# Kernel optimization log

Measured on AMD Instinct MI355X. Metric: run time of the kernel, lower is better.

The kernel has to match this reference:

```python
import jax, jax.numpy as jnp
import numpy as np

B = 32           # graphs in batch
N_PER = 512      # nodes per graph
N = B * N_PER    # 16384 total nodes (block-diagonal batched graph)
E = N * 16       # 262144 edges
D_IN = 128
D_OUT = 128
ASSIGN = 2048    # total clusters = B * K
K = ASSIGN // B  # 64 clusters per graph


def setup_inputs() -> dict:
    key = jax.random.key(0)
    ks = jax.random.split(key, 6)
    h = jax.random.normal(ks[0], (N, D_IN), jnp.float32)
    # edges confined within each graph -> block-diagonal batched adjacency
    gid = jnp.repeat(jnp.arange(B), E // B)
    edge_src = (jax.random.randint(ks[1], (E,), 0, N_PER) + gid * N_PER).astype(jnp.int32)
    edge_dst = (jax.random.randint(ks[2], (E,), 0, N_PER) + gid * N_PER).astype(jnp.int32)
    # GraphSage NodeApply linears: Linear(2*in, out)
    stdv_f = 1.0 / np.sqrt(2 * D_IN)
    W_feat = jax.random.uniform(ks[3], (2 * D_IN, D_OUT), jnp.float32, -stdv_f, stdv_f)
    b_feat = jnp.zeros((D_OUT,), jnp.float32)
    W_pool = jax.random.uniform(ks[4], (2 * D_IN, ASSIGN), jnp.float32, -stdv_f, stdv_f)
    b_pool = jnp.zeros((ASSIGN,), jnp.float32)
    return {"h": h, "W_feat": W_feat, "b_feat": b_feat,
            "W_pool": W_pool, "b_pool": b_pool,
            "edge_src": edge_src, "edge_dst": edge_dst}


def _graphsage(h, W, b, src, dst):
    # mean aggregation over in-neighbors (dropout=0, batch_norm off)
    msg = jax.ops.segment_sum(h[src], dst, num_segments=N)          # [N, d_in]
    deg = jax.ops.segment_sum(jnp.ones((src.shape[0],), h.dtype), dst, num_segments=N)
    h_neigh = msg / jnp.maximum(deg, 1.0)[:, None]
    bundle = jnp.concatenate([h, h_neigh], axis=1) @ W + b          # [N, d_out]
    # F.normalize(p=2, dim=1) then activation, as in GraphSage NodeApply
    norm = jnp.linalg.norm(bundle, axis=1, keepdims=True)
    bundle = bundle / jnp.maximum(norm, 1e-12)
    return jax.nn.relu(bundle)


def _forward(h, W_feat, b_feat, W_pool, b_pool, src, dst):
    feat = _graphsage(h, W_feat, b_feat, src, dst)       # [N, D_OUT]
    assign = _graphsage(h, W_pool, b_pool, src, dst)     # [N, ASSIGN]
    # block-diagonal mask: node i of graph g may only assign to g's K clusters
    gid_n = jnp.arange(N) // N_PER                       # [N]
    gid_c = jnp.arange(ASSIGN) // K                      # [ASSIGN]
    mask = (gid_n[:, None] == gid_c[None, :]).astype(jnp.float32)
    # masked_softmax with memory_efficient=False
    s = jax.nn.softmax(assign * mask, axis=-1) * mask
    s = s / (s.sum(axis=-1, keepdims=True) + 1e-13)      # [N, ASSIGN]
    h_new = s.T @ feat                                   # [ASSIGN, D_OUT]
    # adj_new = S^T A S without densifying A: (A S)[dst] += S[src]
    a_s = jax.ops.segment_sum(s[src], dst, num_segments=N)
    adj_new = s.T @ a_s                                  # [ASSIGN, ASSIGN]
    return adj_new, h_new


def reference(h, W_feat, b_feat, W_pool, b_pool, edge_src, edge_dst):
    return _forward(h, W_feat, b_feat, W_pool, b_pool, edge_src, edge_dst)
```

## Files before the change

### kernel.cpp

```cpp
#include <hip/hip_runtime.h>

#define NB   32
#define NPER 512
#define NN   16384
#define EE   262144
#define DD   128
#define AS   2048
#define KC   64

using short8   = __attribute__((ext_vector_type(8))) short;
using floatx4  = __attribute__((ext_vector_type(4))) float;
using ushort4v = __attribute__((ext_vector_type(4))) unsigned short;

typedef __attribute__((address_space(3))) unsigned int lds_u32;
typedef const __attribute__((address_space(1))) unsigned int gbl_u32;

static __device__ __forceinline__ void gload16(const unsigned short* g, unsigned short* l) {
    __builtin_amdgcn_global_load_lds((gbl_u32*)g, (lds_u32*)l, 16, 0, 0);
}
static __device__ __forceinline__ float bits2f(unsigned int u) {
    union { unsigned int i; float f; } z; z.i = u << 16; return z.f;
}
static __device__ __forceinline__ unsigned short f2b(float x) {
    union { float f; unsigned int u; } v; v.f = x;
    unsigned int r = v.u + 0x7fffu + ((v.u >> 16) & 1u);
    return (unsigned short)(r >> 16);
}
static __device__ __forceinline__ unsigned short f2b_exact(float x) {
    union { float f; unsigned int u; } v; v.f = x;
    return (unsigned short)(v.u >> 16);
}

union PrepSMem {
    unsigned short fT[128 * 136];
    float tl[32][33];
    struct { unsigned short glA[4096]; unsigned short glB[4096]; float gcred[4]; } gg;
};
__global__ void prep_kernel(const float* __restrict__ h, unsigned short* __restrict__ bundle,
                            unsigned short* __restrict__ hT, const int* __restrict__ esrc,
                            const int* __restrict__ edst, unsigned int* __restrict__ Acnt,
                            const float* __restrict__ Wf, const float* __restrict__ Wp,
                            const float* __restrict__ bp,
                            unsigned short* __restrict__ WfT, unsigned short* __restrict__ WpT,
                            float* __restrict__ Gf, float* __restrict__ uF,
                            float* __restrict__ cF) {
    __shared__ PrepSMem sm;
    int b = blockIdx.x, t = threadIdx.x;
    if (b < 32) {
        int ks = b >> 2, ti = (b >> 1) & 1, tj = b & 1;
        int wv = t >> 6, lane = t & 63;
        int mw = wv >> 1, nw = wv & 1, q = lane >> 4, lm = lane & 15;
        int swz = q ^ ((lm >> 1) & 3);
        floatx4 acc[4][4];
#pragma unroll
        for (int mi = 0; mi < 4; mi++)
#pragma unroll
            for (int ni = 0; ni < 4; ni++) acc[mi][ni] = (floatx4)0.f;
        for (int ki = 0; ki < 8; ki++) {
            int k0 = ks * 256 + ki * 32;
#pragma unroll
            for (int half = 0; half < 2; half++) {
                int u = t + 256 * half;
                int row = u >> 2, c = u & 3;
                int cs = c ^ ((row >> 1) & 3);
                const float4* sa = reinterpret_cast<const float4*>(
                    Wp + (size_t)(ti * 128 + row) * 2048 + k0 + c * 8);
                float4 v0 = sa[0], v1 = sa[1];
                ushort4v p0 = { f2b(v0.x), f2b(v0.y), f2b(v0.z), f2b(v0.w) };
                ushort4v p1 = { f2b(v1.x), f2b(v1.y), f2b(v1.z), f2b(v1.w) };
                *reinterpret_cast<ushort4v*>(&sm.gg.glA[(row * 4 + cs) * 8]) = p0;
                *reinterpret_cast<ushort4v*>(&sm.gg.glA[(row * 4 + cs) * 8 + 4]) = p1;
                const float4* sb = reinterpret_cast<const float4*>(
                    Wp + (size_t)(tj * 128 + row) * 2048 + k0 + c * 8);
                float4 w0 = sb[0], w1 = sb[1];
                ushort4v q0 = { f2b(w0.x), f2b(w0.y), f2b(w0.z), f2b(w0.w) };
                ushort4v q1 = { f2b(w1.x), f2b(w1.y), f2b(w1.z), f2b(w1.w) };
                *reinterpret_cast<ushort4v*>(&sm.gg.glB[(row * 4 + cs) * 8]) = q0;
                *reinterpret_cast<ushort4v*>(&sm.gg.glB[(row * 4 + cs) * 8 + 4]) = q1;
            }
            __syncthreads();
            short8 aF[4], bF[4];
#pragma unroll
            for (int mi = 0; mi < 4; mi++)
                aF[mi] = *reinterpret_cast<const short8*>(&sm.gg.glA[((64 * mw + 16 * mi + lm) * 4 + swz) * 8]);
#pragma unroll
            for (int ni = 0; ni < 4; ni++)
                bF[ni] = *reinterpret_cast<const short8*>(&sm.gg.glB[((64 * nw + 16 * ni + lm) * 4 + swz) * 8]);
#pragma unroll
            for (int mi = 0; mi < 4; mi++)
#pragma unroll
                for (int ni = 0; ni < 4; ni++)
                    acc[mi][ni] = __builtin_amdgcn_mfma_f32_16x16x32_bf16(aF[mi], bF[ni], acc[mi][ni], 0, 0, 0);
            __syncthreads();
        }
#pragma unroll
        for (int mi = 0; mi < 4; mi++)
#pragma unroll
            for (int ni = 0; ni < 4; ni++)
#pragma unroll
                for (int r = 0; r < 4; r++)
                    atomicAdd(&Gf[(size_t)(ti * 128 + 64 * mw + 16 * mi + 4 * q + r) * 256 +
                                  tj * 128 + 64 * nw + 16 * ni + lm], acc[mi][ni][r]);
        if (tj == 0) {
            int row = t >> 1, jh = t & 1;
            const float4* wr = reinterpret_cast<const float4*>(
                Wp + (size_t)(ti * 128 + row) * 2048 + ks * 256 + jh * 128);
            const float4* br = reinterpret_cast<const float4*>(bp + ks * 256 + jh * 128);
            float s = 0.f;
#pragma unroll 8
            for (int j = 0; j < 32; j++) {
                float4 a = wr[j], c = br[j];
                s += a.x * c.x + a.y * c.y + a.z * c.z + a.w * c.w;
            }
            s += __shfl_xor(s, 1, 64);
            if (jh == 0) atomicAdd(&uF[ti * 128 + row], s);
        }
        if (b == 0) {
            float s = 0.f;
            for (int j = t; j < 2048; j += 256) { float v = bp[j]; s += v * v; }
#pragma unroll
            for (int d = 1; d < 64; d <<= 1) s += __shfl_xor(s, d, 64);
            if (lane == 0) sm.gg.gcred[wv] = s;
            __syncthreads();
            if (t == 0) atomicAdd(cF, sm.gg.gcred[0] + sm.gg.gcred[1] + sm.gg.gcred[2] + sm.gg.gcred[3]);
        }
    } else if (b < 160) {
        int node0 = (b - 32) * 128;
        int r = t >> 1, hf = t & 1;
        const float4* h4 = reinterpret_cast<const float4*>(h + (size_t)(node0 + r) * 128 + hf * 64);
        unsigned short* bo = bundle + (size_t)(node0 + r) * 256 + hf * 64;
#pragma unroll
        for (int i = 0; i < 16; i++) {
            float4 v = h4[i];
            ushort4v o = { f2b(v.x), f2b(v.y), f2b(v.z), f2b(v.w) };
            *reinterpret_cast<ushort4v*>(bo + 4 * i) = o;
            int c = hf * 64 + 4 * i;
            sm.fT[(c + 0) * 136 + r] = o.x;
            sm.fT[(c + 1) * 136 + r] = o.y;
            sm.fT[(c + 2) * 136 + r] = o.z;
            sm.fT[(c + 3) * 136 + r] = o.w;
        }
        __syncthreads();
        int c = t >> 1, nh = t & 1;
        const uint4* src = reinterpret_cast<const uint4*>(&sm.fT[c * 136 + nh * 64]);
        uint4* dst = reinterpret_cast<uint4*>(hT + (size_t)c * NN + node0 + nh * 64);
#pragma unroll
        for (int i = 0; i < 8; i++) dst[i] = src[i];
    } else if (b < 1184) {
        int e = (b - 160) * 256 + t;
        int d = edst[e], sl = esrc[e] & 511;
        int idx = d * 512 + sl;
        atomicAdd(&Acnt[idx >> 2], 1u << (8 * (idx & 3)));
    } else {
        int tb = b - 1184;
        int bx = tb % 68, by = tb / 68;
        int tx = t & 31, ty = t >> 5;
        const float* in; unsigned short* out; int C, cb;
        if (bx < DD / 32) { in = Wf; out = WfT; C = DD; cb = bx; }
        else              { in = Wp; out = WpT; C = AS; cb = bx - DD / 32; }
        int c0 = cb * 32, r0 = by * 32;
        for (int i = 0; i < 4; i++)
            sm.tl[ty + 8 * i][tx] = in[(size_t)(r0 + ty + 8 * i) * C + c0 + tx];
        __syncthreads();
        for (int i = 0; i < 4; i++)
            out[(size_t)(c0 + ty + 8 * i) * 256 + r0 + tx] = f2b(sm.tl[tx][ty + 8 * i]);
    }
}

__global__ __launch_bounds__(256) void agg_h_mfma_kernel(
    const unsigned int* __restrict__ Acnt, const unsigned short* __restrict__ hT,
    unsigned short* __restrict__ bundle, unsigned short* __restrict__ Aadj,
    const float* __restrict__ Gf, unsigned short* __restrict__ Gb) {
    __shared__ alignas(16) unsigned short lA[64 * 512];
    __shared__ float rs[64];
    int tid = threadIdx.x, bx = blockIdx.x;
    if (bx >= 256) {
        int base = (bx - 256) * 16384;
        for (int i = 0; i < 16; i++) {
            int idx = base + i * 1024 + tid * 4;
            float4 v = *reinterpret_cast<const float4*>(Gf + idx);
            ushort4v o = { f2b(v.x), f2b(v.y), f2b(v.z), f2b(v.w) };
            *reinterpret_cast<ushort4v*>(&Gb[idx]) = o;
        }
        return;
    }
    int r0 = bx * 64, g = bx >> 3;
    int wv = tid >> 6, lane = tid & 63, q = lane >> 4, lm = lane & 15;
    int mw = wv >> 1, nw = wv & 1;
    if (tid < 64) rs[tid] = 0.f;
    __syncthreads();
#pragma unroll
    for (int j = 0; j < 8; j++) {
        int ub = tid + 256 * j;
        int row = ub >> 5, kb = ub & 31;
        uint4 w = reinterpret_cast<const uint4*>(Acnt)[(size_t)(r0 + row) * 32 + kb];
        unsigned int wa[4] = { w.x, w.y, w.z, w.w };
        unsigned short ob[16];
        float sum = 0.f;
#pragma unroll
        for (int i = 0; i < 4; i++) {
#pragma unroll
            for (int bb = 0; bb < 4; bb++) {
                float fv = (float)((wa[i] >> (8 * bb)) & 0xffu);
                sum += fv;
                ob[4 * i + bb] = f2b_exact(fv);
            }
        }
        atomicAdd(&rs[row], sum);
        uint4* gdst = reinterpret_cast<uint4*>(&Aadj[(size_t)(r0 + row) * 512 + kb * 16]);
        gdst[0] = *reinterpret_cast<const uint4*>(&ob[0]);
        gdst[1] = *reinterpret_cast<const uint4*>(&ob[8]);
#pragma unroll
        for (int jj = 0; jj < 2; jj++) {
            int pos = (kb * 2 + jj) ^ (row & 7);
            *reinterpret_cast<uint4*>(&lA[(row * 64 + pos) * 8]) =
                *reinterpret_cast<const uint4*>(&ob[8 * jj]);
        }
    }
    floatx4 acc[2][4];
#pragma unroll
    for (int mt = 0; mt < 2; mt++)
#pragma unroll
        for (int nt = 0; nt < 4; nt++) acc[mt][nt] = (floatx4)0.f;
    __syncthreads();
    const unsigned short* Bb = hT + (size_t)(64 * nw + lm) * NN + g * 512 + (q << 3);
    short8 bF[2][4];
#pragma unroll
    for (int nt = 0; nt < 4; nt++)
        bF[0][nt] = *reinterpret_cast<const short8*>(Bb + (size_t)16 * nt * NN);
    for (int ki = 0; ki < 16; ki++) {
        if (ki < 15) {
#pragma unroll
            for (int nt = 0; nt < 4; nt++)
                bF[(ki + 1) & 1][nt] =
                    *reinterpret_cast<const short8*>(Bb + (size_t)16 * nt * NN + (ki + 1) * 32);
        }
        short8 aF[2];
        int swz = (4 * ki + q) ^ (lm & 7);
#pragma unroll
        for (int mt = 0; mt < 2; mt++)
            aF[mt] = *reinterpret_cast<const short8*>(&lA[((32 * mw + 16 * mt + lm) * 64 + swz) * 8]);
#pragma unroll
        for (int mt = 0; mt < 2; mt++)
#pragma unroll
            for (int nt = 0; nt < 4; nt++)
                acc[mt][nt] = __builtin_amdgcn_mfma_f32_16x16x32_bf16(aF[mt], bF[ki & 1][nt],
                                                                      acc[mt][nt], 0, 0, 0);
    }
#pragma unroll
    for (int mt = 0; mt < 2; mt++)
#pragma unroll
        for (int r = 0; r < 4; r++) {
            int row = 32 * mw + 16 * mt + 4 * q + r;
            float inv = 1.0f / fmaxf(rs[row], 1.0f);
#pragma unroll
            for (int nt = 0; nt < 4; nt++)
                bundle[(size_t)(r0 + row) * 256 + 128 + 64 * nw + 16 * nt + lm] =
                    f2b(acc[mt][nt][r] * inv);
        }
}

union FPSMem {
    struct { unsigned short lA[4096]; unsigned short lB[4096]; float red[256]; } feat;
    struct { unsigned short lA[16384]; float raw[4352]; float ssq[256]; float rn[64];
             float uL[256]; } pool;
};
__global__ __launch_bounds__(256) void featpool_kernel(
    const unsigned short* __restrict__ bundle, const unsigned short* __restrict__ WfT,
    const unsigned short* __restrict__ WpT, const unsigned short* __restrict__ Gb,
    const float* __restrict__ bfe, const float* __restrict__ bp,
    const float* __restrict__ uF, const float* __restrict__ cF,
    unsigned short* __restrict__ featT, unsigned short* __restrict__ sT) {
    __shared__ FPSMem sm;
    int tid = threadIdx.x, b = blockIdx.x;
    if (b < 128) {
        int r0 = b * 128;
        int wv = tid >> 6, lane = tid & 63;
        int mw = wv >> 1, nw = wv & 1, q = lane >> 4, lm = lane & 15;
        int rowS0 = tid >> 2,         cS0 = (tid & 3) ^ ((rowS0 >> 1) & 3);
        int rowS1 = (tid + 256) >> 2, cS1 = ((tid + 256) & 3) ^ ((rowS1 >> 1) & 3);
        int swz = q ^ ((lm >> 1) & 3);
        floatx4 acc[4][4];
#pragma unroll
        for (int mi = 0; mi < 4; mi++)
#pragma unroll
            for (int ni = 0; ni < 4; ni++) acc[mi][ni] = (floatx4)0.f;
        for (int k0 = 0; k0 < 256; k0 += 32) {
            gload16(bundle + (size_t)(r0 + rowS0) * 256 + k0 + 8 * cS0, &sm.feat.lA[tid * 8]);
            gload16(bundle + (size_t)(r0 + rowS1) * 256 + k0 + 8 * cS1, &sm.feat.lA[(tid + 256) * 8]);
            gload16(WfT + (size_t)rowS0 * 256 + k0 + 8 * cS0, &sm.feat.lB[tid * 8]);
            gload16(WfT + (size_t)rowS1 * 256 + k0 + 8 * cS1, &sm.feat.lB[(tid + 256) * 8]);
            __syncthreads();
            short8 aF[4], bF[4];
#pragma unroll
            for (int mi = 0; mi < 4; mi++)
                aF[mi] = *reinterpret_cast<const short8*>(&sm.feat.lA[((64 * mw + 16 * mi + lm) * 4 + swz) * 8]);
#pragma unroll
            for (int ni = 0; ni < 4; ni++)
                bF[ni] = *reinterpret_cast<const short8*>(&sm.feat.lB[((64 * nw + 16 * ni + lm) * 4 + swz) * 8]);
#pragma unroll
            for (int mi = 0; mi < 4; mi++)
#pragma unroll
                for (int ni = 0; ni < 4; ni++)
                    acc[mi][ni] = __builtin_amdgcn_mfma_f32_16x16x32_bf16(aF[mi], bF[ni], acc[mi][ni], 0, 0, 0);
            __syncthreads();
        }
#pragma unroll
        for (int ni = 0; ni < 4; ni++) {
            float bv = bfe[64 * nw + 16 * ni + lm];
#pragma unroll
            for (int mi = 0; mi < 4; mi++)
#pragma unroll
                for (int r = 0; r < 4; r++) acc[mi][ni][r] += bv;
        }
#pragma unroll
        for (int mi = 0; mi < 4; mi++)
#pragma unroll
            for (int r = 0; r < 4; r++) {
                float p = 0.f;
#pragma unroll
                for (int ni = 0; ni < 4; ni++) p += acc[mi][ni][r] * acc[mi][ni][r];
                p += __shfl_xor(p, 1, 64);
                p += __shfl_xor(p, 2, 64);
                p += __shfl_xor(p, 4, 64);
                p += __shfl_xor(p, 8, 64);
                if (lm == 0) sm.feat.red[nw * 128 + 64 * mw + 16 * mi + 4 * q + r] = p;
            }
        __syncthreads();
#pragma unroll
        for (int mi = 0; mi < 4; mi++) {
            float rrn[4];
#pragma unroll
            for (int r = 0; r < 4; r++) {
                int rl = 64 * mw + 16 * mi + 4 * q + r;
                rrn[r] = 1.0f / fmaxf(sqrtf(sm.feat.red[rl] + sm.feat.red[128 + rl]), 1e-12f);
            }
#pragma unroll
            for (int ni = 0; ni < 4; ni++) {
                int col = 64 * nw + 16 * ni + lm;
                ushort4v pk = { f2b(fmaxf(acc[mi][ni][0] * rrn[0], 0.f)),
                                f2b(fmaxf(acc[mi][ni][1] * rrn[1], 0.f)),
                                f2b(fmaxf(acc[mi][ni][2] * rrn[2], 0.f)),
                                f2b(fmaxf(acc[mi][ni][3] * rrn[3], 0.f)) };
                *reinterpret_cast<ushort4v*>(
                    &featT[(size_t)col * NN + r0 + 64 * mw + 16 * mi + 4 * q]) = pk;
            }
        }
    } else {
        int bx = b - 128;
        int r0 = bx * 64, g = bx >> 3;
        int wv = tid >> 6, lane = tid & 63, q = lane >> 4, lm = lane & 15;
#pragma unroll
        for (int j = 0; j < 8; j++) {
            int u = tid + 256 * j;
            int row = u >> 5;
            int chunk = (u & 31) ^ (row & 7);
            gload16(bundle + (size_t)(r0 + row) * 256 + chunk * 8, &sm.pool.lA[u * 8]);
        }
        sm.pool.uL[tid] = uF[tid];
        __syncthreads();
        {
            const unsigned short* Bb = Gb + ((size_t)(wv * 64 + lm) << 8) + (q << 3);
            short8 bF[2][4];
#pragma unroll
            for (int ni = 0; ni < 4; ni++)
                bF[0][ni] = *reinterpret_cast<const short8*>(Bb + (ni << 12));
            floatx4 acc[4][4];
#pragma unroll
            for (int mi = 0; mi < 4; mi++)
#pragma unroll
                for (int ni = 0; ni < 4; ni++) acc[mi][ni] = (floatx4)0.f;
#pragma unroll
            for (int k = 0; k < 8; k++) {
                if (k < 7) {
#pragma unroll
                    for (int ni = 0; ni < 4; ni++)
                        bF[(k + 1) & 1][ni] =
                            *reinterpret_cast<const short8*>(Bb + (ni << 12) + ((k + 1) << 5));
                }
                short8 aF[4];
                int swz = (4 * k + q) ^ (lm & 7);
#pragma unroll
                for (int mi = 0; mi < 4; mi++)
                    aF[mi] = *reinterpret_cast<const short8*>(&sm.pool.lA[((16 * mi + lm) * 32 + swz) * 8]);
#pragma unroll
                for (int mi = 0; mi < 4; mi++)
#pragma unroll
                    for (int ni = 0; ni < 4; ni++)
                        acc[mi][ni] = __builtin_amdgcn_mfma_f32_16x16x32_bf16(aF[mi], bF[k & 1][ni],
                                                                              acc[mi][ni], 0, 0, 0);
            }
            float uc[4];
#pragma unroll
            for (int ni = 0; ni < 4; ni++) uc[ni] = sm.pool.uL[64 * wv + 16 * ni + lm];
#pragma unroll
            for (int mi = 0; mi < 4; mi++)
#pragma unroll
                for (int r = 0; r < 4; r++) {
                    int row = 16 * mi + 4 * q + r;
                    float p = 0.f;
#pragma unroll
                    for (int ni = 0; ni < 4; ni++) {
                        int col = 64 * wv + 16 * ni + lm;
                        int cu = (col >> 3) ^ (row & 7);
                        float xv = bits2f((unsigned int)sm.pool.lA[(row * 32 + cu) * 8 + (col & 7)]);
                        p += (acc[mi][ni][r] + 2.f * uc[ni]) * xv;
                    }
                    p += __shfl_xor(p, 1, 64);
                    p += __shfl_xor(p, 2, 64);
                    p += __shfl_xor(p, 4, 64);
                    p += __shfl_xor(p, 8, 64);
                    if (lm == 0) sm.pool.ssq[wv * 64 + row] = p;
                }
        }
        {
            const unsigned short* Bb2 = WpT + (size_t)(g * KC + 16 * wv + lm) * 256 + (q << 3);
            short8 b2[2];
            b2[0] = *reinterpret_cast<const short8*>(Bb2);
            floatx4 acc2[4];
#pragma unroll
            for (int mi = 0; mi < 4; mi++) acc2[mi] = (floatx4)0.f;
#pragma unroll
            for (int k = 0; k < 8; k++) {
                if (k < 7) b2[(k + 1) & 1] = *reinterpret_cast<const short8*>(Bb2 + ((k + 1) << 5));
                short8 aF[4];
                int swz = (4 * k + q) ^ (lm & 7);
#pragma unroll
                for (int mi = 0; mi < 4; mi++)
                    aF[mi] = *reinterpret_cast<const short8*>(&sm.pool.lA[((16 * mi + lm) * 32 + swz) * 8]);
#pragma unroll
                for (int mi = 0; mi < 4; mi++)
                    acc2[mi] = __builtin_amdgcn_mfma_f32_16x16x32_bf16(aF[mi], b2[k & 1], acc2[mi], 0, 0, 0);
            }
            float bv = bp[g * KC + 16 * wv + lm];
#pragma unroll
            for (int mi = 0; mi < 4; mi++)
#pragma unroll
                for (int r = 0; r < 4; r++)
                    sm.pool.raw[(16 * mi + 4 * q + r) * 68 + 16 * wv + lm] = acc2[mi][r] + bv;
        }
        __syncthreads();
        if (tid < 64)
            sm.pool.rn[tid] = 1.0f / fmaxf(sqrtf(sm.pool.ssq[tid] + sm.pool.ssq[64 + tid] +
                                           sm.pool.ssq[128 + tid] + sm.pool.ssq[192 + tid] + cF[0]), 1e-12f);
        __syncthreads();
        {
            int row = tid >> 2, j = tid & 3;
            int nloc = ((bx & 7) << 6) + row;
            float rn = sm.pool.rn[row];
            float v[16];
            float mx = -1e30f;
#pragma unroll
            for (int c4 = 0; c4 < 4; c4++) {
                float4 rv = *reinterpret_cast<const float4*>(&sm.pool.raw[row * 68 + 16 * j + 4 * c4]);
                v[4 * c4 + 0] = fmaxf(rv.x * rn, 0.f);
                v[4 * c4 + 1] = fmaxf(rv.y * rn, 0.f);
                v[4 * c4 + 2] = fmaxf(rv.z * rn, 0.f);
                v[4 * c4 + 3] = fmaxf(rv.w * rn, 0.f);
            }
#pragma unroll
            for (int c = 0; c < 16; c++) mx = fmaxf(mx, v[c]);
            mx = fmaxf(mx, __shfl_xor(mx, 1, 64));
            mx = fmaxf(mx, __shfl_xor(mx, 2, 64));
            float z = 0.f;
#pragma unroll
            for (int c = 0; c < 16; c++) { v[c] = __expf(v[c] - mx); z += v[c]; }
            z += __shfl_xor(z, 1, 64);
            z += __shfl_xor(z, 2, 64);
            float iz = 1.0f / z;
#pragma unroll
            for (int c4 = 0; c4 < 4; c4++) {
                size_t tb = (size_t)(g * KC + 16 * j + 4 * c4) * NPER + nloc;
                sT[tb] = f2b(v[4 * c4 + 0] * iz);
                sT[tb + NPER] = f2b(v[4 * c4 + 1] * iz);
                sT[tb + 2 * NPER] = f2b(v[4 * c4 + 2] * iz);
                sT[tb + 3 * NPER] = f2b(v[4 * c4 + 3] * iz);
            }
        }
    }
}

__global__ __launch_bounds__(256) void as_mfma_kernel(
    const unsigned short* __restrict__ sT, const unsigned short* __restrict__ Aadj,
    unsigned short* __restrict__ asT) {
    __shared__ alignas(16) unsigned short lS[64 * 512];
    int tid = threadIdx.x, bx = blockIdx.x;
    int g = bx >> 1, half = bx & 1;
    int wv = tid >> 6, lane = tid & 63, q = lane >> 4, lm = lane & 15;
#pragma unroll
    for (int j = 0; j < 16; j++) {
        int u = tid + 256 * j;
        int row = u >> 6, cu = (u & 63) ^ (row & 7);
        gload16(sT + (size_t)(g * KC + row) * NPER + cu * 8, &lS[u * 8]);
    }
    floatx4 acc[4][4];
#pragma unroll
    for (int mi = 0; mi < 4; mi++)
#pragma unroll
        for (int nt = 0; nt < 4; nt++) acc[mi][nt] = (floatx4)0.f;
    __syncthreads();
    int dbase = half * 256 + wv * 64;
    const unsigned short* Bb = Aadj + (size_t)(g * 512 + dbase + lm) * 512 + (q << 3);
    short8 bF[2][4];
#pragma unroll
    for (int nt = 0; nt < 4; nt++)
        bF[0][nt] = *reinterpret_cast<const short8*>(Bb + (size_t)16 * nt * 512);
    for (int ki = 0; ki < 16; ki++) {
        if (ki < 15) {
#pragma unroll
            for (int nt = 0; nt < 4; nt++)
                bF[(ki + 1) & 1][nt] =
                    *reinterpret_cast<const short8*>(Bb + (size_t)16 * nt * 512 + (ki + 1) * 32);
        }
        short8 aF[4];
        int swz = (4 * ki + q) ^ (lm & 7);
#pragma unroll
        for (int mi = 0; mi < 4; mi++)
            aF[mi] = *reinterpret_cast<const short8*>(&lS[((16 * mi + lm) * 64 + swz) * 8]);
#pragma unroll
        for (int mi = 0; mi < 4; mi++)
#pragma unroll
            for (int nt = 0; nt < 4; nt++)
                acc[mi][nt] = __builtin_amdgcn_mfma_f32_16x16x32_bf16(aF[mi], bF[ki & 1][nt],
                                                                      acc[mi][nt], 0, 0, 0);
    }
#pragma unroll
    for (int mi = 0; mi < 4; mi++)
#pragma unroll
        for (int r = 0; r < 4; r++) {
            int row = 16 * mi + 4 * q + r;
#pragma unroll
            for (int nt = 0; nt < 4; nt++)
                asT[(size_t)(g * KC + row) * NPER + dbase + 16 * nt + lm] = f2b(acc[mi][nt][r]);
        }
}

__global__ __launch_bounds__(256) void hnew_adj2_kernel(
    const unsigned short* __restrict__ sT, const unsigned short* __restrict__ featT,
    const unsigned short* __restrict__ asT, float* __restrict__ adjf,
    float* __restrict__ hnewf) {
    __shared__ alignas(16) unsigned short lS[1024 * 8];
    __shared__ alignas(16) unsigned short lF[2048 * 8];
    __shared__ alignas(16) unsigned short lAS[1024 * 8];
    int tid = threadIdx.x, b = blockIdx.x;
    if (b >= 32) {
        uint4 z = { 0u, 0u, 0u, 0u };
        for (int row = b - 32; row < AS; row += 224) {
            int g = row >> 6;
            uint4* out = reinterpret_cast<uint4*>(adjf + (size_t)row * AS);
            for (int i = tid; i < 512; i += 256)
                if (i < g * 16 || i >= g * 16 + 16) out[i] = z;
        }
        return;
    }
    int g = b;
    int wv = tid >> 6, lane = tid & 63, q = lane >> 4, lm = lane & 15;
    bool isH = (wv < 2);
    floatx4 accH[4][4];
    floatx4 accA[4][2];
#pragma unroll
    for (int mi = 0; mi < 4; mi++) {
#pragma unroll
        for (int ni = 0; ni < 4; ni++) accH[mi][ni] = (floatx4)0.f;
#pragma unroll
        for (int ni = 0; ni < 2; ni++) accA[mi][ni] = (floatx4)0.f;
    }
    for (int ks = 0; ks < 4; ks++) {
#pragma unroll
        for (int j = 0; j < 4; j++) {
            int u = tid + 256 * j;
            int row = u >> 4, cu = (u & 15) ^ (row & 15);
            gload16(sT + (size_t)(g * KC + row) * NPER + ks * 128 + cu * 8, &lS[u * 8]);
        }
#pragma unroll
        for (int j = 0; j < 8; j++) {
            int u = tid + 256 * j;
            int row = u >> 4, cu = (u & 15) ^ (row & 15);
            gload16(featT + (size_t)row * NN + g * NPER + ks * 128 + cu * 8, &lF[u * 8]);
        }
#pragma unroll
        for (int j = 0; j < 4; j++) {
            int u = tid + 256 * j;
            int row = u >> 4, cu = (u & 15) ^ (row & 15);
            gload16(asT + (size_t)(g * KC + row) * NPER + ks * 128 + cu * 8, &lAS[u * 8]);
        }
        __syncthreads();
#pragma unroll
        for (int kk = 0; kk < 4; kk++) {
            short8 aF[4];
#pragma unroll
            for (int mi = 0; mi < 4; mi++)
                aF[mi] = *reinterpret_cast<const short8*>(
                    &lS[((16 * mi + lm) * 16 + ((4 * kk + q) ^ lm)) * 8]);
            if (isH) {
                short8 bF[4];
#pragma unroll
                for (int ni = 0; ni < 4; ni++)
                    bF[ni] = *reinterpret_cast<const short8*>(
                        &lF[((64 * wv + 16 * ni + lm) * 16 + ((4 * kk + q) ^ lm)) * 8]);
#pragma unroll
                for (int mi = 0; mi < 4; mi++)
#pragma unroll
                    for (int ni = 0; ni < 4; ni++)
                        accH[mi][ni] = __builtin_amdgcn_mfma_f32_16x16x32_bf16(aF[mi], bF[ni],
                                                                               accH[mi][ni], 0, 0, 0);
            } else {
                short8 bF[2];
#pragma unroll
                for (int ni = 0; ni < 2; ni++)
                    bF[ni] = *reinterpret_cast<const short8*>(
                        &lAS[((32 * (wv - 2) + 16 * ni + lm) * 16 + ((4 * kk + q) ^ lm)) * 8]);
#pragma unroll
                for (int mi = 0; mi < 4; mi++)
#pragma unroll
                    for (int ni = 0; ni < 2; ni++)
                        accA[mi][ni] = __builtin_amdgcn_mfma_f32_16x16x32_bf16(aF[mi], bF[ni],
                                                                               accA[mi][ni], 0, 0, 0);
            }
        }
        __syncthreads();
    }
    if (isH) {
#pragma unroll
        for (int mi = 0; mi < 4; mi++)
#pragma unroll
            for (int ni = 0; ni < 4; ni++)
#pragma unroll
                for (int r = 0; r < 4; r++)
                    hnewf[(size_t)(g * KC + 16 * mi + 4 * q + r) * DD +
                          64 * wv + 16 * ni + lm] = accH[mi][ni][r];
    } else {
#pragma unroll
        for (int mi = 0; mi < 4; mi++)
#pragma unroll
            for (int ni = 0; ni < 2; ni++)
#pragma unroll
                for (int r = 0; r < 4; r++)
                    adjf[(size_t)(g * KC + 16 * mi + 4 * q + r) * AS +
                         g * KC + 32 * (wv - 2) + 16 * ni + lm] = accA[mi][ni][r];
    }
}

extern "C" void kernel_launch(void* const* d_in, const int* in_sizes, int n_in,
                              void* d_out, int out_size, void* d_ws, size_t ws_size,
                              hipStream_t stream) {
    const float* h   = (const float*)d_in[0];
    const float* Wf  = (const float*)d_in[1];
    const float* bfe = (const float*)d_in[2];
    const float* Wp  = (const float*)d_in[3];
    const float* bp  = (const float*)d_in[4];
    const int* esrc  = (const int*)d_in[5];
    const int* edst  = (const int*)d_in[6];

    float* adjf  = (float*)d_out;
    float* hnewf = adjf + (size_t)AS * AS;

    unsigned short* bundle = (unsigned short*)d_ws;
    unsigned short* WfT   = bundle + (size_t)NN * 256;
    unsigned short* WpT   = WfT + 128 * 256;
    unsigned short* sT    = WpT + (size_t)AS * 256;
    unsigned short* asT   = sT + (size_t)NN * KC;
    unsigned short* featT = asT + (size_t)NN * KC;
    unsigned short* hT    = featT + (size_t)DD * NN;
    unsigned short* Aadj  = hT + (size_t)DD * NN;
    unsigned int* Acnt = (unsigned int*)(Aadj + (size_t)NN * 512);
    float* Gf = (float*)(Acnt + (size_t)NN * 128);
    float* uF = Gf + 65536;
    float* cF = uF + 256;
    unsigned short* Gb = (unsigned short*)(cF + 4);

    hipMemsetAsync(Acnt, 0, (size_t)NN * 512 + (65536 + 256 + 4) * sizeof(float), stream);

    prep_kernel<<<1728, 256, 0, stream>>>(h, bundle, hT, esrc, edst, Acnt,
                                          Wf, Wp, bp, WfT, WpT, Gf, uF, cF);
    agg_h_mfma_kernel<<<260, 256, 0, stream>>>(Acnt, hT, bundle, Aadj, Gf, Gb);
    featpool_kernel<<<384, 256, 0, stream>>>(bundle, WfT, WpT, Gb, bfe, bp, uF, cF, featT, sT);
    as_mfma_kernel<<<NB * 2, 256, 0, stream>>>(sT, Aadj, asT);
    hnew_adj2_kernel<<<256, 256, 0, stream>>>(sT, featT, asT, adjf, hnewf);
}
```

Measured before the change: 162.9 us.

## Convert Gram matrix to bf16 on the fly and split as_mfma K across waves

Drops the separate fp32-to-bf16 conversion of the Gram matrix from the aggregation kernel; the pool branch now loads fp32 Gf directly and packs it to bf16 in registers while the MFMAs run. Separately, the as_mfma kernel now launches twice as many blocks, and within each block the waves split the 512-long reduction in half, combining partial sums through LDS before writing. This removes an extra pass over the buffer and raises occupancy in a kernel that launched only 64 blocks. The cost is twice the global load bytes for the B operand, extra conversion work inside the pool loop, and an added LDS reduction with barriers.

```diff
diff --git a/kernel.cpp b/kernel.cpp
--- a/kernel.cpp
+++ b/kernel.cpp
@@ -1,4 +1,5 @@
 #include <hip/hip_runtime.h>
+#include <hip/hip_bf16.h>
 
 #define NB   32
 #define NPER 512
@@ -29,6 +30,18 @@
 static __device__ __forceinline__ unsigned short f2b_exact(float x) {
     union { float f; unsigned int u; } v; v.f = x;
     return (unsigned short)(v.u >> 16);
+}
+static __device__ __forceinline__ short8 pk8(float4 a, float4 b) {
+    union { short8 s; unsigned int u[4]; } o;
+    __hip_bfloat162 t0 = __float22bfloat162_rn(make_float2(a.x, a.y));
+    __hip_bfloat162 t1 = __float22bfloat162_rn(make_float2(a.z, a.w));
+    __hip_bfloat162 t2 = __float22bfloat162_rn(make_float2(b.x, b.y));
+    __hip_bfloat162 t3 = __float22bfloat162_rn(make_float2(b.z, b.w));
+    o.u[0] = *reinterpret_cast<unsigned int*>(&t0);
+    o.u[1] = *reinterpret_cast<unsigned int*>(&t1);
+    o.u[2] = *reinterpret_cast<unsigned int*>(&t2);
+    o.u[3] = *reinterpret_cast<unsigned int*>(&t3);
+    return o.s;
 }
 
 union PrepSMem {
@@ -169,21 +182,10 @@
 
 __global__ __launch_bounds__(256) void agg_h_mfma_kernel(
     const unsigned int* __restrict__ Acnt, const unsigned short* __restrict__ hT,
-    unsigned short* __restrict__ bundle, unsigned short* __restrict__ Aadj,
-    const float* __restrict__ Gf, unsigned short* __restrict__ Gb) {
+    unsigned short* __restrict__ bundle, unsigned short* __restrict__ Aadj) {
     __shared__ alignas(16) unsigned short lA[64 * 512];
     __shared__ float rs[64];
     int tid = threadIdx.x, bx = blockIdx.x;
-    if (bx >= 256) {
-        int base = (bx - 256) * 16384;
-        for (int i = 0; i < 16; i++) {
-            int idx = base + i * 1024 + tid * 4;
-            float4 v = *reinterpret_cast<const float4*>(Gf + idx);
-            ushort4v o = { f2b(v.x), f2b(v.y), f2b(v.z), f2b(v.w) };
-            *reinterpret_cast<ushort4v*>(&Gb[idx]) = o;
-        }
-        return;
-    }
     int r0 = bx * 64, g = bx >> 3;
     int wv = tid >> 6, lane = tid & 63, q = lane >> 4, lm = lane & 15;
     int mw = wv >> 1, nw = wv & 1;
@@ -267,7 +269,7 @@
 };
 __global__ __launch_bounds__(256) void featpool_kernel(
     const unsigned short* __restrict__ bundle, const unsigned short* __restrict__ WfT,
-    const unsigned short* __restrict__ WpT, const unsigned short* __restrict__ Gb,
+    const unsigned short* __restrict__ WpT, const float* __restrict__ Gf,
     const float* __restrict__ bfe, const float* __restrict__ bp,
     const float* __restrict__ uF, const float* __restrict__ cF,
     unsigned short* __restrict__ featT, unsigned short* __restrict__ sT) {
@@ -360,11 +362,16 @@
         sm.pool.uL[tid] = uF[tid];
         __syncthreads();
         {
-            const unsigned short* Bb = Gb + ((size_t)(wv * 64 + lm) << 8) + (q << 3);
+            const float* Bf = Gf + (size_t)(wv * 64 + lm) * 256 + (q << 3);
             short8 bF[2][4];
-#pragma unroll
-            for (int ni = 0; ni < 4; ni++)
-                bF[0][ni] = *reinterpret_cast<const short8*>(Bb + (ni << 12));
+            float4 tA[4], tB[4];
+#pragma unroll
+            for (int ni = 0; ni < 4; ni++) {
+                tA[ni] = *reinterpret_cast<const float4*>(Bf + (ni << 12));
+                tB[ni] = *reinterpret_cast<const float4*>(Bf + (ni << 12) + 4);
+            }
+#pragma unroll
+            for (int ni = 0; ni < 4; ni++) bF[0][ni] = pk8(tA[ni], tB[ni]);
             floatx4 acc[4][4];
 #pragma unroll
             for (int mi = 0; mi < 4; mi++)
@@ -374,9 +381,10 @@
             for (int k = 0; k < 8; k++) {
                 if (k < 7) {
 #pragma unroll
-                    for (int ni = 0; ni < 4; ni++)
-                        bF[(k + 1) & 1][ni] =
-                            *reinterpret_cast<const short8*>(Bb + (ni << 12) + ((k + 1) << 5));
+                    for (int ni = 0; ni < 4; ni++) {
+                        tA[ni] = *reinterpret_cast<const float4*>(Bf + (ni << 12) + ((k + 1) << 5));
+                        tB[ni] = *reinterpret_cast<const float4*>(Bf + (ni << 12) + ((k + 1) << 5) + 4);
+                    }
                 }
                 short8 aF[4];
                 int swz = (4 * k + q) ^ (lm & 7);
@@ -389,6 +397,10 @@
                     for (int ni = 0; ni < 4; ni++)
                         acc[mi][ni] = __builtin_amdgcn_mfma_f32_16x16x32_bf16(aF[mi], bF[k & 1][ni],
                                                                               acc[mi][ni], 0, 0, 0);
+                if (k < 7) {
+#pragma unroll
+                    for (int ni = 0; ni < 4; ni++) bF[(k + 1) & 1][ni] = pk8(tA[ni], tB[ni]);
+                }
             }
             float uc[4];
 #pragma unroll
@@ -485,8 +497,9 @@
     unsigned short* __restrict__ asT) {
     __shared__ alignas(16) unsigned short lS[64 * 512];
     int tid = threadIdx.x, bx = blockIdx.x;
-    int g = bx >> 1, half = bx & 1;
+    int g = bx >> 2, dq = bx & 3;
     int wv = tid >> 6, lane = tid & 63, q = lane >> 4, lm = lane & 15;
+    int ds = wv & 1, kh = wv >> 1;
 #pragma unroll
     for (int j = 0; j < 16; j++) {
         int u = tid + 256 * j;
@@ -499,21 +512,21 @@
 #pragma unroll
         for (int nt = 0; nt < 4; nt++) acc[mi][nt] = (floatx4)0.f;
     __syncthreads();
-    int dbase = half * 256 + wv * 64;
-    const unsigned short* Bb = Aadj + (size_t)(g * 512 + dbase + lm) * 512 + (q << 3);
+    int dbase = dq * 128 + ds * 64;
+    const unsigned short* Bb = Aadj + (size_t)(g * 512 + dbase + lm) * 512 + kh * 256 + (q << 3);
     short8 bF[2][4];
 #pragma unroll
     for (int nt = 0; nt < 4; nt++)
         bF[0][nt] = *reinterpret_cast<const short8*>(Bb + (size_t)16 * nt * 512);
-    for (int ki = 0; ki < 16; ki++) {
-        if (ki < 15) {
+    for (int ki = 0; ki < 8; ki++) {
+        if (ki < 7) {
 #pragma unroll
             for (int nt = 0; nt < 4; nt++)
                 bF[(ki + 1) & 1][nt] =
                     *reinterpret_cast<const short8*>(Bb + (size_t)16 * nt * 512 + (ki + 1) * 32);
         }
         short8 aF[4];
-        int swz = (4 * ki + q) ^ (lm & 7);
+        int swz = (32 * kh + 4 * ki + q) ^ (lm & 7);
 #pragma unroll
         for (int mi = 0; mi < 4; mi++)
             aF[mi] = *reinterpret_cast<const short8*>(&lS[((16 * mi + lm) * 64 + swz) * 8]);
@@ -524,15 +537,33 @@
                 acc[mi][nt] = __builtin_amdgcn_mfma_f32_16x16x32_bf16(aF[mi], bF[ki & 1][nt],
                                                                       acc[mi][nt], 0, 0, 0);
     }
-#pragma unroll
-    for (int mi = 0; mi < 4; mi++)
-#pragma unroll
-        for (int r = 0; r < 4; r++) {
-            int row = 16 * mi + 4 * q + r;
-#pragma unroll
-            for (int nt = 0; nt < 4; nt++)
-                asT[(size_t)(g * KC + row) * NPER + dbase + 16 * nt + lm] = f2b(acc[mi][nt][r]);
-        }
+    __syncthreads();
+    float* comb = reinterpret_cast<float*>(lS);
+    if (kh == 1) {
+#pragma unroll
+        for (int mi = 0; mi < 4; mi++)
+#pragma unroll
+            for (int r = 0; r < 4; r++) {
+                int row = 16 * mi + 4 * q + r;
+#pragma unroll
+                for (int nt = 0; nt < 4; nt++)
+                    comb[ds * 4096 + row * 64 + 16 * nt + lm] = acc[mi][nt][r];
+            }
+    }
+    __syncthreads();
+    if (kh == 0) {
+#pragma unroll
+        for (int mi = 0; mi < 4; mi++)
+#pragma unroll
+            for (int r = 0; r < 4; r++) {
+                int row = 16 * mi + 4 * q + r;
+#pragma unroll
+                for (int nt = 0; nt < 4; nt++) {
+                    float v = acc[mi][nt][r] + comb[ds * 4096 + row * 64 + 16 * nt + lm];
+                    asT[(size_t)(g * KC + row) * NPER + dbase + 16 * nt + lm] = f2b(v);
+                }
+            }
+    }
 }
 
 __global__ __launch_bounds__(256) void hnew_adj2_kernel(
@@ -667,14 +698,13 @@
     float* Gf = (float*)(Acnt + (size_t)NN * 128);
     float* uF = Gf + 65536;
     float* cF = uF + 256;
-    unsigned short* Gb = (unsigned short*)(cF + 4);
 
     hipMemsetAsync(Acnt, 0, (size_t)NN * 512 + (65536 + 256 + 4) * sizeof(float), stream);
 
     prep_kernel<<<1728, 256, 0, stream>>>(h, bundle, hT, esrc, edst, Acnt,
                                           Wf, Wp, bp, WfT, WpT, Gf, uF, cF);
-    agg_h_mfma_kernel<<<260, 256, 0, stream>>>(Acnt, hT, bundle, Aadj, Gf, Gb);
-    featpool_kernel<<<384, 256, 0, stream>>>(bundle, WfT, WpT, Gb, bfe, bp, uF, cF, featT, sT);
-    as_mfma_kernel<<<NB * 2, 256, 0, stream>>>(sT, Aadj, asT);
+    agg_h_mfma_kernel<<<256, 256, 0, stream>>>(Acnt, hT, bundle, Aadj);
+    featpool_kernel<<<384, 256, 0, stream>>>(bundle, WfT, WpT, Gf, bfe, bp, uF, cF, featT, sT);
+    as_mfma_kernel<<<NB * 4, 256, 0, stream>>>(sT, Aadj, asT);
     hnew_adj2_kernel<<<256, 256, 0, stream>>>(sT, featT, asT, adjf, hnewf);
 }
```

Result: no change. 164.2 us (+0.8%).
